# Optimization experiments

Measured on AMD Instinct MI355X. Metric: run time of the kernel, lower is better.

The kernel has to match this reference:

```python
import jax, jax.numpy as jnp
import numpy as np
import math

EMBED = 512
HEADS = 2
HEAD_DIM = EMBED // HEADS
EPS = 1e-5

def layer_norm(x, g, b):
    mu = jnp.mean(x, axis=-1, keepdims=True)
    var = jnp.var(x, axis=-1, keepdims=True)
    return (x - mu) * jax.lax.rsqrt(var + EPS) * g + b

def setup_inputs() -> dict:
    key = jax.random.key(0)
    ks = jax.random.split(key, 16)
    s = 0.02
    inp = {
        "text_embeds": jax.random.normal(ks[0], (128, 32, EMBED), jnp.float32),
        "video_embeds": jax.random.normal(ks[1], (64, 12, EMBED), jnp.float32),
        "ln1_g": jnp.ones((EMBED,), jnp.float32),
        "ln1_b": jnp.zeros((EMBED,), jnp.float32),
        "Wq": jax.random.normal(ks[2], (EMBED, EMBED), jnp.float32) * s,
        "bq": jnp.zeros((EMBED,), jnp.float32),
        "Wk": jax.random.normal(ks[3], (EMBED, EMBED), jnp.float32) * s,
        "bk": jnp.zeros((EMBED,), jnp.float32),
        "Wv": jax.random.normal(ks[4], (EMBED, EMBED), jnp.float32) * s,
        "bv": jnp.zeros((EMBED,), jnp.float32),
        "Wo": jax.random.normal(ks[5], (EMBED, EMBED), jnp.float32) * s,
        "bo": jnp.zeros((EMBED,), jnp.float32),
        "Wl": jax.random.normal(ks[6], (EMBED, EMBED), jnp.float32) * s,
        "bl": jnp.zeros((EMBED,), jnp.float32),
        "ln2_g": jnp.ones((EMBED,), jnp.float32),
        "ln2_b": jnp.zeros((EMBED,), jnp.float32),
        "ln3_g": jnp.ones((EMBED,), jnp.float32),
        "ln3_b": jnp.zeros((EMBED,), jnp.float32),
    }
    return inp

def reference(text_embeds, video_embeds, ln1_g, ln1_b, Wq, bq, Wk, bk, Wv, bv,
              Wo, bo, Wl, bl, ln2_g, ln2_b, ln3_g, ln3_b):
    # shared layer_norm1 on both modalities
    t = layer_norm(text_embeds, ln1_g, ln1_b)    # [T, Nw, E]
    vd = layer_norm(video_embeds, ln1_g, ln1_b)  # [V, F, E]
    T, Nw, _ = t.shape
    V, Fr, _ = vd.shape
    q = (t @ Wq.T + bq).reshape(T, Nw, HEADS, HEAD_DIM)   # bthd
    k = (vd @ Wk.T + bk).reshape(V, Fr, HEADS, HEAD_DIM)  # avhd
    v = (vd @ Wv.T + bv).reshape(V, Fr, HEADS, HEAD_DIM)  # avhd
    # cross-modal outer-product attention logits: [V, T, H, F, Nw]
    logits = jnp.einsum('avhd,bthd->abhvt', k, q) / math.sqrt(HEAD_DIM)
    weights = jax.nn.softmax(logits, axis=3)  # softmax over frames
    attn = jnp.einsum('avhd,abhvt->abhtd', v, weights)  # [V, T, H, Nw, D]
    attn = attn.transpose(0, 1, 3, 2, 4).reshape(V, T, Nw, EMBED)
    attn = attn.mean(axis=0)                    # [T, Nw, E]
    o = attn @ Wo.T + bo
    o = layer_norm(o, ln2_g, ln2_b)
    lin = o @ Wl.T + bl  # dropout is identity in eval mode
    out = layer_norm(o + lin, ln3_g, ln3_b)
    return out
```

## Files before the change

kernel.cpp:

```cpp
#include <hip/hip_runtime.h>
#include <math.h>

#define EMBED 512
#define HD 256
#define FR 12
#define NV 64
#define NT_TOK 4096
#define NV_TOK 768

typedef __attribute__((ext_vector_type(8))) short short8;
typedef __attribute__((ext_vector_type(4))) float f32x4;

__device__ __forceinline__ unsigned short f2bf(float f) {
  unsigned int u = __float_as_uint(f);
  u += 0x7FFFu + ((u >> 16) & 1u);
  return (unsigned short)(u >> 16);
}
__device__ __forceinline__ float bf2f(unsigned short h) {
  return __uint_as_float(((unsigned int)h) << 16);
}
__device__ __forceinline__ void async_cp16(void* lds, const void* g) {
  __builtin_amdgcn_global_load_lds(
      (const __attribute__((address_space(1))) void*)g,
      (__attribute__((address_space(3))) void*)lds, 16, 0, 0);
}

__global__ __launch_bounds__(256) void ln_kernel(
    const float* __restrict__ x, const float* __restrict__ res,
    const float* __restrict__ g, const float* __restrict__ b,
    float* __restrict__ outf, unsigned short* __restrict__ outb) {
  int row = blockIdx.x;
  int t = threadIdx.x;
  const float* xr = x + (size_t)row * EMBED;
  float v0 = xr[t];
  float v1 = xr[t + 256];
  if (res != nullptr) {
    const float* rr = res + (size_t)row * EMBED;
    v0 += rr[t];
    v1 += rr[t + 256];
  }
  float s = v0 + v1;
  float s2 = v0 * v0 + v1 * v1;
  #pragma unroll
  for (int off = 32; off > 0; off >>= 1) {
    s += __shfl_down(s, off, 64);
    s2 += __shfl_down(s2, off, 64);
  }
  __shared__ float ss[4], ss2[4];
  __shared__ float mean_s, rstd_s;
  int wid = t >> 6;
  if ((t & 63) == 0) { ss[wid] = s; ss2[wid] = s2; }
  __syncthreads();
  if (t == 0) {
    float a = ss[0] + ss[1] + ss[2] + ss[3];
    float a2 = ss2[0] + ss2[1] + ss2[2] + ss2[3];
    float mean = a * (1.0f / EMBED);
    float var = a2 * (1.0f / EMBED) - mean * mean;
    mean_s = mean;
    rstd_s = rsqrtf(var + 1e-5f);
  }
  __syncthreads();
  float mean = mean_s, rstd = rstd_s;
  float y0 = (v0 - mean) * rstd * g[t] + b[t];
  float y1 = (v1 - mean) * rstd * g[t + 256] + b[t + 256];
  if (outf != nullptr) {
    float* orow = outf + (size_t)row * EMBED;
    orow[t] = y0;
    orow[t + 256] = y1;
  }
  if (outb != nullptr) {
    unsigned short* orow = outb + (size_t)row * EMBED;
    orow[t] = f2bf(y0);
    orow[t + 256] = f2bf(y1);
  }
}

template <bool OUT_BF, bool BIAS>
__global__ __launch_bounds__(256) void gemm_mfma(
    const unsigned short* __restrict__ A, int lda, long AzS,
    const unsigned short* __restrict__ B, int ldb, long BzS,
    const float* __restrict__ bias, void* __restrict__ Cv, int ldc, long CzS,
    int K) {
  __shared__ __align__(16) unsigned short As[64 * 64];
  __shared__ __align__(16) unsigned short Bs[64 * 64];
  int tid = threadIdx.x;
  int w = tid >> 6, lane = tid & 63;
  int m0 = blockIdx.x * 64, n0 = blockIdx.y * 64;
  const unsigned short* Ab = A + (size_t)blockIdx.z * AzS;
  const unsigned short* Bb = B + (size_t)blockIdx.z * BzS;
  int wm = (w >> 1) * 32, wn = (w & 1) * 32;
  int lr = lane & 15, quad = lane >> 4;

  int s0 = lane, s1 = 64 + lane;
  int row0 = (w << 4) + (s0 >> 3), c0l = s0 & 7, c0g = c0l ^ (row0 & 7);
  int row1 = (w << 4) + (s1 >> 3), c1l = s1 & 7, c1g = c1l ^ (row1 & 7);

  f32x4 acc[2][2] = {};
  for (int k0 = 0; k0 < K; k0 += 64) {
    __syncthreads();
    async_cp16(&As[row0 * 64 + c0l * 8], Ab + (size_t)(m0 + row0) * lda + k0 + c0g * 8);
    async_cp16(&As[row1 * 64 + c1l * 8], Ab + (size_t)(m0 + row1) * lda + k0 + c1g * 8);
    async_cp16(&Bs[row0 * 64 + c0l * 8], Bb + (size_t)(n0 + row0) * ldb + k0 + c0g * 8);
    async_cp16(&Bs[row1 * 64 + c1l * 8], Bb + (size_t)(n0 + row1) * ldb + k0 + c1g * 8);
    __syncthreads();
    #pragma unroll
    for (int kk = 0; kk < 2; ++kk) {
      int sw = ((kk * 4 + quad) ^ (lr & 7)) * 8;
      short8 a0 = *(const short8*)&As[(wm + lr) * 64 + sw];
      short8 a1 = *(const short8*)&As[(wm + 16 + lr) * 64 + sw];
      short8 b0 = *(const short8*)&Bs[(wn + lr) * 64 + sw];
      short8 b1 = *(const short8*)&Bs[(wn + 16 + lr) * 64 + sw];
      acc[0][0] = __builtin_amdgcn_mfma_f32_16x16x32_bf16(a0, b0, acc[0][0], 0, 0, 0);
      acc[0][1] = __builtin_amdgcn_mfma_f32_16x16x32_bf16(a0, b1, acc[0][1], 0, 0, 0);
      acc[1][0] = __builtin_amdgcn_mfma_f32_16x16x32_bf16(a1, b0, acc[1][0], 0, 0, 0);
      acc[1][1] = __builtin_amdgcn_mfma_f32_16x16x32_bf16(a1, b1, acc[1][1], 0, 0, 0);
    }
  }
  long cz = (long)blockIdx.z * CzS;
  #pragma unroll
  for (int im = 0; im < 2; ++im) {
    #pragma unroll
    for (int in = 0; in < 2; ++in) {
      int col = n0 + wn + in * 16 + lr;
      float bv = BIAS ? bias[col] : 0.0f;
      int rbase = m0 + wm + im * 16 + quad * 4;
      #pragma unroll
      for (int r = 0; r < 4; ++r) {
        float v = acc[im][in][r] + bv;
        if (OUT_BF)
          ((unsigned short*)Cv)[cz + (size_t)(rbase + r) * ldc + col] = f2bf(v);
        else
          ((float*)Cv)[cz + (size_t)(rbase + r) * ldc + col] = v;
      }
    }
  }
}

__global__ __launch_bounds__(256) void cvt5_kernel(
    const float* __restrict__ w0, const float* __restrict__ w1,
    const float* __restrict__ w2, const float* __restrict__ w3,
    const float* __restrict__ w4, unsigned short* __restrict__ out) {
  int i = blockIdx.x * 256 + threadIdx.x;
  const float* srcs[5] = {w0, w1, w2, w3, w4};
  const float* src = srcs[i >> 16];
  float4 v = ((const float4*)src)[i & 65535];
  uint2 o;
  o.x = (unsigned)f2bf(v.x) | ((unsigned)f2bf(v.y) << 16);
  o.y = (unsigned)f2bf(v.z) | ((unsigned)f2bf(v.w) << 16);
  ((uint2*)out)[i] = o;
}

__global__ __launch_bounds__(256) void softmax12_kernel(unsigned short* __restrict__ S) {
  int gi = blockIdx.x * 256 + threadIdx.x;
  uint2* p = (uint2*)(S + (size_t)gi * 12);
  uint2 u0 = p[0], u1 = p[1], u2 = p[2];
  float v[12];
  v[0] = bf2f(u0.x & 0xffff); v[1] = bf2f(u0.x >> 16);
  v[2] = bf2f(u0.y & 0xffff); v[3] = bf2f(u0.y >> 16);
  v[4] = bf2f(u1.x & 0xffff); v[5] = bf2f(u1.x >> 16);
  v[6] = bf2f(u1.y & 0xffff); v[7] = bf2f(u1.y >> 16);
  v[8] = bf2f(u2.x & 0xffff); v[9] = bf2f(u2.x >> 16);
  v[10] = bf2f(u2.y & 0xffff); v[11] = bf2f(u2.y >> 16);
  float m = -1e30f;
  #pragma unroll
  for (int f = 0; f < FR; ++f) { v[f] *= 0.0625f; m = fmaxf(m, v[f]); }
  float s = 0.f;
  #pragma unroll
  for (int f = 0; f < FR; ++f) { v[f] = __expf(v[f] - m); s += v[f]; }
  float inv = (1.0f / NV) / s;
  unsigned short w[12];
  #pragma unroll
  for (int f = 0; f < FR; ++f) w[f] = f2bf(v[f] * inv);
  uint2 o0, o1, o2;
  o0.x = (unsigned)w[0] | ((unsigned)w[1] << 16);
  o0.y = (unsigned)w[2] | ((unsigned)w[3] << 16);
  o1.x = (unsigned)w[4] | ((unsigned)w[5] << 16);
  o1.y = (unsigned)w[6] | ((unsigned)w[7] << 16);
  o2.x = (unsigned)w[8] | ((unsigned)w[9] << 16);
  o2.y = (unsigned)w[10] | ((unsigned)w[11] << 16);
  p[0] = o0; p[1] = o1; p[2] = o2;
}

__global__ __launch_bounds__(256) void transpose_kernel(
    const unsigned short* __restrict__ V, unsigned short* __restrict__ Vt) {
  __shared__ unsigned short tile[32][34];
  int x = threadIdx.x & 31, y = threadIdx.x >> 5;
  int t0 = blockIdx.x * 32, n0 = blockIdx.y * 32;
  #pragma unroll
  for (int i = 0; i < 4; ++i)
    tile[y + i * 8][x] = V[(size_t)(t0 + y + i * 8) * EMBED + n0 + x];
  __syncthreads();
  #pragma unroll
  for (int i = 0; i < 4; ++i)
    Vt[(size_t)(n0 + y + i * 8) * NV_TOK + t0 + x] = tile[x][y + i * 8];
}

extern "C" void kernel_launch(void* const* d_in, const int* in_sizes, int n_in,
                              void* d_out, int out_size, void* d_ws, size_t ws_size,
                              hipStream_t stream) {
  (void)in_sizes; (void)n_in; (void)out_size; (void)ws_size;
  const float* text  = (const float*)d_in[0];
  const float* video = (const float*)d_in[1];
  const float* ln1_g = (const float*)d_in[2];
  const float* ln1_b = (const float*)d_in[3];
  const float* Wq = (const float*)d_in[4];
  const float* bq = (const float*)d_in[5];
  const float* Wk = (const float*)d_in[6];
  const float* bk = (const float*)d_in[7];
  const float* Wv = (const float*)d_in[8];
  const float* bv = (const float*)d_in[9];
  const float* Wo = (const float*)d_in[10];
  const float* bo = (const float*)d_in[11];
  const float* Wl = (const float*)d_in[12];
  const float* bl = (const float*)d_in[13];
  const float* ln2_g = (const float*)d_in[14];
  const float* ln2_b = (const float*)d_in[15];
  const float* ln3_g = (const float*)d_in[16];
  const float* ln3_b = (const float*)d_in[17];
  float* out = (float*)d_out;

  char* base = (char*)d_ws;
  unsigned short* Wbf   = (unsigned short*)base;
  unsigned short* Wq_bf = Wbf + 0 * 262144;
  unsigned short* Wk_bf = Wbf + 1 * 262144;
  unsigned short* Wv_bf = Wbf + 2 * 262144;
  unsigned short* Wo_bf = Wbf + 3 * 262144;
  unsigned short* Wl_bf = Wbf + 4 * 262144;
  unsigned short* Vt    = (unsigned short*)(base + 2621440);
  char* big = base + 3407872;
  unsigned short* Q_bf   = (unsigned short*)(big + 0);
  unsigned short* K_bf   = (unsigned short*)(big + 4194304);
  unsigned short* S      = (unsigned short*)(big + 4980736);
  unsigned short* tn_bf  = (unsigned short*)(big + 17563648);
  unsigned short* vn_bf  = (unsigned short*)(big + 21757952);
  unsigned short* V_bf   = (unsigned short*)(big + 22544384);
  unsigned short* att_bf = (unsigned short*)(big + 17563648);
  float*          Ob     = (float*)(big + 4980736);
  float*          o2f    = (float*)(big + 13369344);
  unsigned short* o2_bf  = (unsigned short*)(big + 21757952);
  float*          lin    = (float*)(big + 0);

  cvt5_kernel<<<1280, 256, 0, stream>>>(Wq, Wk, Wv, Wo, Wl, Wbf);
  ln_kernel<<<NT_TOK, 256, 0, stream>>>(text, nullptr, ln1_g, ln1_b, nullptr, tn_bf);
  ln_kernel<<<NV_TOK, 256, 0, stream>>>(video, nullptr, ln1_g, ln1_b, nullptr, vn_bf);

  gemm_mfma<true, true><<<dim3(64, 8, 1), 256, 0, stream>>>(
      tn_bf, EMBED, 0, Wq_bf, EMBED, 0, bq, Q_bf, EMBED, 0, EMBED);
  gemm_mfma<true, true><<<dim3(12, 8, 1), 256, 0, stream>>>(
      vn_bf, EMBED, 0, Wk_bf, EMBED, 0, bk, K_bf, EMBED, 0, EMBED);
  gemm_mfma<true, true><<<dim3(12, 8, 1), 256, 0, stream>>>(
      vn_bf, EMBED, 0, Wv_bf, EMBED, 0, bv, V_bf, EMBED, 0, EMBED);
  transpose_kernel<<<dim3(24, 16), 256, 0, stream>>>(V_bf, Vt);

  gemm_mfma<true, false><<<dim3(64, 12, 2), 256, 0, stream>>>(
      Q_bf, EMBED, HD, K_bf, EMBED, HD, nullptr, S, NV_TOK, (long)NT_TOK * NV_TOK, HD);
  softmax12_kernel<<<2048, 256, 0, stream>>>(S);
  gemm_mfma<true, false><<<dim3(64, 4, 2), 256, 0, stream>>>(
      S, NV_TOK, (long)NT_TOK * NV_TOK, Vt, NV_TOK, (long)HD * NV_TOK, nullptr,
      att_bf, EMBED, HD, NV_TOK);

  gemm_mfma<false, true><<<dim3(64, 8, 1), 256, 0, stream>>>(
      att_bf, EMBED, 0, Wo_bf, EMBED, 0, bo, Ob, EMBED, 0, EMBED);
  ln_kernel<<<NT_TOK, 256, 0, stream>>>(Ob, nullptr, ln2_g, ln2_b, o2f, o2_bf);
  gemm_mfma<false, true><<<dim3(64, 8, 1), 256, 0, stream>>>(
      o2_bf, EMBED, 0, Wl_bf, EMBED, 0, bl, lin, EMBED, 0, EMBED);
  ln_kernel<<<NT_TOK, 256, 0, stream>>>(o2f, lin, ln3_g, ln3_b, out, nullptr);
}
```

Measured before the change: 183.9 us.

## Fuse prep and QKV launches, write V transposed, enlarge GEMM tiles to 128x64

Merges the weight conversion and both layer norms into one prep kernel, and merges the Q, K and V projections into one grid-partitioned kernel. The V projection now writes its output directly in transposed layout, which removes the separate transpose kernel. All GEMMs move from 64x64 to 128x64 block tiles, so each block reuses its B tile across more rows. The aims are fewer launches and less tile reload traffic, at the cost of fewer blocks per grid and more registers per thread.

```diff
diff --git a/kernel.cpp b/kernel.cpp
--- a/kernel.cpp
+++ b/kernel.cpp
@@ -11,13 +11,13 @@
 typedef __attribute__((ext_vector_type(8))) short short8;
 typedef __attribute__((ext_vector_type(4))) float f32x4;
 
-__device__ __forceinline__ unsigned short f2bf(float f) {
+__device__ __forceinline__ unsigned int f2bf(float f) {
   unsigned int u = __float_as_uint(f);
   u += 0x7FFFu + ((u >> 16) & 1u);
-  return (unsigned short)(u >> 16);
-}
-__device__ __forceinline__ float bf2f(unsigned short h) {
-  return __uint_as_float(((unsigned int)h) << 16);
+  return u >> 16;
+}
+__device__ __forceinline__ float bf2f(unsigned int h) {
+  return __uint_as_float(h << 16);
 }
 __device__ __forceinline__ void async_cp16(void* lds, const void* g) {
   __builtin_amdgcn_global_load_lds(
@@ -25,20 +25,154 @@
       (__attribute__((address_space(3))) void*)lds, 16, 0, 0);
 }
 
-__global__ __launch_bounds__(256) void ln_kernel(
-    const float* __restrict__ x, const float* __restrict__ res,
+__device__ __forceinline__ void gemm_core(
+    const unsigned short* __restrict__ Ab, int lda,
+    const unsigned short* __restrict__ Bb, int ldb,
+    int m0, int n0, int K,
+    unsigned short* As, unsigned short* Bs, f32x4 acc[4][2]) {
+  int tid = threadIdx.x;
+  int w = tid >> 6, lane = tid & 63;
+  int lr = lane & 15, quad = lane >> 4;
+  int wm = (w >> 1) * 64, wn = (w & 1) * 32;
+  int rowA[4], cgA[4], rowB[2], cgB[2];
+  #pragma unroll
+  for (int i = 0; i < 4; ++i) {
+    int s = tid + i * 256;
+    rowA[i] = s >> 3;
+    cgA[i] = (s & 7) ^ (rowA[i] & 7);
+  }
+  #pragma unroll
+  for (int i = 0; i < 2; ++i) {
+    int s = tid + i * 256;
+    rowB[i] = s >> 3;
+    cgB[i] = (s & 7) ^ (rowB[i] & 7);
+  }
+  for (int k0 = 0; k0 < K; k0 += 64) {
+    __syncthreads();
+    #pragma unroll
+    for (int i = 0; i < 4; ++i)
+      async_cp16(&As[(tid + i * 256) * 8],
+                 Ab + (size_t)(m0 + rowA[i]) * lda + k0 + cgA[i] * 8);
+    #pragma unroll
+    for (int i = 0; i < 2; ++i)
+      async_cp16(&Bs[(tid + i * 256) * 8],
+                 Bb + (size_t)(n0 + rowB[i]) * ldb + k0 + cgB[i] * 8);
+    __syncthreads();
+    #pragma unroll
+    for (int kk = 0; kk < 2; ++kk) {
+      int sw = ((kk * 4 + quad) ^ (lr & 7)) * 8;
+      short8 b0 = *(const short8*)&Bs[(wn + lr) * 64 + sw];
+      short8 b1 = *(const short8*)&Bs[(wn + 16 + lr) * 64 + sw];
+      #pragma unroll
+      for (int i = 0; i < 4; ++i) {
+        short8 a = *(const short8*)&As[(wm + i * 16 + lr) * 64 + sw];
+        acc[i][0] = __builtin_amdgcn_mfma_f32_16x16x32_bf16(a, b0, acc[i][0], 0, 0, 0);
+        acc[i][1] = __builtin_amdgcn_mfma_f32_16x16x32_bf16(a, b1, acc[i][1], 0, 0, 0);
+      }
+    }
+  }
+}
+
+template <bool OUT_BF, bool BIAS>
+__global__ __launch_bounds__(256) void gemm128(
+    const unsigned short* __restrict__ A, int lda, long AzS,
+    const unsigned short* __restrict__ B, int ldb, long BzS,
+    const float* __restrict__ bias, void* __restrict__ Cv, int ldc, long CzS,
+    int K) {
+  __shared__ __align__(16) unsigned short As[128 * 64];
+  __shared__ __align__(16) unsigned short Bs[64 * 64];
+  f32x4 acc[4][2] = {};
+  const unsigned short* Ab = A + (size_t)blockIdx.z * AzS;
+  const unsigned short* Bb = B + (size_t)blockIdx.z * BzS;
+  int m0 = blockIdx.x * 128, n0 = blockIdx.y * 64;
+  gemm_core(Ab, lda, Bb, ldb, m0, n0, K, As, Bs, acc);
+  int w = threadIdx.x >> 6, lane = threadIdx.x & 63;
+  int lr = lane & 15, quad = lane >> 4;
+  int wm = (w >> 1) * 64, wn = (w & 1) * 32;
+  long cz = (long)blockIdx.z * CzS;
+  #pragma unroll
+  for (int j = 0; j < 2; ++j) {
+    int col = n0 + wn + j * 16 + lr;
+    float bv = BIAS ? bias[col] : 0.0f;
+    #pragma unroll
+    for (int i = 0; i < 4; ++i) {
+      int rbase = m0 + wm + i * 16 + quad * 4;
+      #pragma unroll
+      for (int r = 0; r < 4; ++r) {
+        float v = acc[i][j][r] + bv;
+        if (OUT_BF)
+          ((unsigned short*)Cv)[cz + (size_t)(rbase + r) * ldc + col] =
+              (unsigned short)f2bf(v);
+        else
+          ((float*)Cv)[cz + (size_t)(rbase + r) * ldc + col] = v;
+      }
+    }
+  }
+}
+
+__global__ __launch_bounds__(256) void qkv_kernel(
+    const unsigned short* __restrict__ tn, const unsigned short* __restrict__ vn,
+    const unsigned short* __restrict__ Wq, const unsigned short* __restrict__ Wk,
+    const unsigned short* __restrict__ Wv,
+    const float* __restrict__ bq, const float* __restrict__ bk,
+    const float* __restrict__ bv,
+    unsigned short* __restrict__ Q, unsigned short* __restrict__ Kout,
+    unsigned short* __restrict__ Vt) {
+  __shared__ __align__(16) unsigned short As[128 * 64];
+  __shared__ __align__(16) unsigned short Bs[64 * 64];
+  int bid = blockIdx.x;
+  const unsigned short *Ap, *Bp;
+  const float* bias;
+  unsigned short* outp = nullptr;
+  int m0, n0, mode;
+  if (bid < 256) {
+    Ap = tn; Bp = Wq; bias = bq; outp = Q;
+    m0 = (bid >> 3) * 128; n0 = (bid & 7) * 64; mode = 0;
+  } else if (bid < 304) {
+    int i = bid - 256;
+    Ap = vn; Bp = Wk; bias = bk; outp = Kout;
+    m0 = (i >> 3) * 128; n0 = (i & 7) * 64; mode = 0;
+  } else {
+    int i = bid - 304;
+    Ap = vn; Bp = Wv; bias = bv;
+    m0 = (i >> 3) * 128; n0 = (i & 7) * 64; mode = 1;
+  }
+  f32x4 acc[4][2] = {};
+  gemm_core(Ap, EMBED, Bp, EMBED, m0, n0, EMBED, As, Bs, acc);
+  int w = threadIdx.x >> 6, lane = threadIdx.x & 63;
+  int lr = lane & 15, quad = lane >> 4;
+  int wm = (w >> 1) * 64, wn = (w & 1) * 32;
+  #pragma unroll
+  for (int j = 0; j < 2; ++j) {
+    int col = n0 + wn + j * 16 + lr;
+    float bvv = bias[col];
+    #pragma unroll
+    for (int i = 0; i < 4; ++i) {
+      int rbase = m0 + wm + i * 16 + quad * 4;
+      if (mode == 0) {
+        #pragma unroll
+        for (int r = 0; r < 4; ++r)
+          outp[(size_t)(rbase + r) * EMBED + col] =
+              (unsigned short)f2bf(acc[i][j][r] + bvv);
+      } else {
+        ushort4 pk;
+        pk.x = (unsigned short)f2bf(acc[i][j][0] + bvv);
+        pk.y = (unsigned short)f2bf(acc[i][j][1] + bvv);
+        pk.z = (unsigned short)f2bf(acc[i][j][2] + bvv);
+        pk.w = (unsigned short)f2bf(acc[i][j][3] + bvv);
+        *(ushort4*)&Vt[(size_t)col * NV_TOK + rbase] = pk;
+      }
+    }
+  }
+}
+
+__device__ __forceinline__ void ln_row(
+    const float* __restrict__ xr, const float* __restrict__ rr,
     const float* __restrict__ g, const float* __restrict__ b,
     float* __restrict__ outf, unsigned short* __restrict__ outb) {
-  int row = blockIdx.x;
   int t = threadIdx.x;
-  const float* xr = x + (size_t)row * EMBED;
-  float v0 = xr[t];
-  float v1 = xr[t + 256];
-  if (res != nullptr) {
-    const float* rr = res + (size_t)row * EMBED;
-    v0 += rr[t];
-    v1 += rr[t + 256];
-  }
+  float v0 = xr[t], v1 = xr[t + 256];
+  if (rr != nullptr) { v0 += rr[t]; v1 += rr[t + 256]; }
   float s = v0 + v1;
   float s2 = v0 * v0 + v1 * v1;
   #pragma unroll
@@ -63,91 +197,49 @@
   float mean = mean_s, rstd = rstd_s;
   float y0 = (v0 - mean) * rstd * g[t] + b[t];
   float y1 = (v1 - mean) * rstd * g[t + 256] + b[t + 256];
-  if (outf != nullptr) {
-    float* orow = outf + (size_t)row * EMBED;
-    orow[t] = y0;
-    orow[t + 256] = y1;
-  }
+  if (outf != nullptr) { outf[t] = y0; outf[t + 256] = y1; }
   if (outb != nullptr) {
-    unsigned short* orow = outb + (size_t)row * EMBED;
-    orow[t] = f2bf(y0);
-    orow[t + 256] = f2bf(y1);
-  }
-}
-
-template <bool OUT_BF, bool BIAS>
-__global__ __launch_bounds__(256) void gemm_mfma(
-    const unsigned short* __restrict__ A, int lda, long AzS,
-    const unsigned short* __restrict__ B, int ldb, long BzS,
-    const float* __restrict__ bias, void* __restrict__ Cv, int ldc, long CzS,
-    int K) {
-  __shared__ __align__(16) unsigned short As[64 * 64];
-  __shared__ __align__(16) unsigned short Bs[64 * 64];
-  int tid = threadIdx.x;
-  int w = tid >> 6, lane = tid & 63;
-  int m0 = blockIdx.x * 64, n0 = blockIdx.y * 64;
-  const unsigned short* Ab = A + (size_t)blockIdx.z * AzS;
-  const unsigned short* Bb = B + (size_t)blockIdx.z * BzS;
-  int wm = (w >> 1) * 32, wn = (w & 1) * 32;
-  int lr = lane & 15, quad = lane >> 4;
-
-  int s0 = lane, s1 = 64 + lane;
-  int row0 = (w << 4) + (s0 >> 3), c0l = s0 & 7, c0g = c0l ^ (row0 & 7);
-  int row1 = (w << 4) + (s1 >> 3), c1l = s1 & 7, c1g = c1l ^ (row1 & 7);
-
-  f32x4 acc[2][2] = {};
-  for (int k0 = 0; k0 < K; k0 += 64) {
-    __syncthreads();
-    async_cp16(&As[row0 * 64 + c0l * 8], Ab + (size_t)(m0 + row0) * lda + k0 + c0g * 8);
-    async_cp16(&As[row1 * 64 + c1l * 8], Ab + (size_t)(m0 + row1) * lda + k0 + c1g * 8);
-    async_cp16(&Bs[row0 * 64 + c0l * 8], Bb + (size_t)(n0 + row0) * ldb + k0 + c0g * 8);
-    async_cp16(&Bs[row1 * 64 + c1l * 8], Bb + (size_t)(n0 + row1) * ldb + k0 + c1g * 8);
-    __syncthreads();
-    #pragma unroll
-    for (int kk = 0; kk < 2; ++kk) {
-      int sw = ((kk * 4 + quad) ^ (lr & 7)) * 8;
-      short8 a0 = *(const short8*)&As[(wm + lr) * 64 + sw];
-      short8 a1 = *(const short8*)&As[(wm + 16 + lr) * 64 + sw];
-      short8 b0 = *(const short8*)&Bs[(wn + lr) * 64 + sw];
-      short8 b1 = *(const short8*)&Bs[(wn + 16 + lr) * 64 + sw];
-      acc[0][0] = __builtin_amdgcn_mfma_f32_16x16x32_bf16(a0, b0, acc[0][0], 0, 0, 0);
-      acc[0][1] = __builtin_amdgcn_mfma_f32_16x16x32_bf16(a0, b1, acc[0][1], 0, 0, 0);
-      acc[1][0] = __builtin_amdgcn_mfma_f32_16x16x32_bf16(a1, b0, acc[1][0], 0, 0, 0);
-      acc[1][1] = __builtin_amdgcn_mfma_f32_16x16x32_bf16(a1, b1, acc[1][1], 0, 0, 0);
-    }
-  }
-  long cz = (long)blockIdx.z * CzS;
-  #pragma unroll
-  for (int im = 0; im < 2; ++im) {
-    #pragma unroll
-    for (int in = 0; in < 2; ++in) {
-      int col = n0 + wn + in * 16 + lr;
-      float bv = BIAS ? bias[col] : 0.0f;
-      int rbase = m0 + wm + im * 16 + quad * 4;
-      #pragma unroll
-      for (int r = 0; r < 4; ++r) {
-        float v = acc[im][in][r] + bv;
-        if (OUT_BF)
-          ((unsigned short*)Cv)[cz + (size_t)(rbase + r) * ldc + col] = f2bf(v);
-        else
-          ((float*)Cv)[cz + (size_t)(rbase + r) * ldc + col] = v;
-      }
-    }
-  }
-}
-
-__global__ __launch_bounds__(256) void cvt5_kernel(
-    const float* __restrict__ w0, const float* __restrict__ w1,
-    const float* __restrict__ w2, const float* __restrict__ w3,
-    const float* __restrict__ w4, unsigned short* __restrict__ out) {
-  int i = blockIdx.x * 256 + threadIdx.x;
-  const float* srcs[5] = {w0, w1, w2, w3, w4};
-  const float* src = srcs[i >> 16];
-  float4 v = ((const float4*)src)[i & 65535];
-  uint2 o;
-  o.x = (unsigned)f2bf(v.x) | ((unsigned)f2bf(v.y) << 16);
-  o.y = (unsigned)f2bf(v.z) | ((unsigned)f2bf(v.w) << 16);
-  ((uint2*)out)[i] = o;
+    outb[t] = (unsigned short)f2bf(y0);
+    outb[t + 256] = (unsigned short)f2bf(y1);
+  }
+}
+
+__global__ __launch_bounds__(256) void ln_kernel(
+    const float* __restrict__ x, const float* __restrict__ res,
+    const float* __restrict__ g, const float* __restrict__ b,
+    float* __restrict__ outf, unsigned short* __restrict__ outb) {
+  size_t row = blockIdx.x;
+  ln_row(x + row * EMBED, res ? res + row * EMBED : nullptr, g, b,
+         outf ? outf + row * EMBED : nullptr,
+         outb ? outb + row * EMBED : nullptr);
+}
+
+__global__ __launch_bounds__(256) void prep_kernel(
+    const float* __restrict__ text, const float* __restrict__ video,
+    const float* __restrict__ g, const float* __restrict__ b,
+    const float* __restrict__ Wq, const float* __restrict__ Wk,
+    const float* __restrict__ Wv, const float* __restrict__ Wo,
+    const float* __restrict__ Wl, unsigned short* __restrict__ Wbf,
+    unsigned short* __restrict__ tn, unsigned short* __restrict__ vn) {
+  int bid = blockIdx.x;
+  if (bid < 1280) {
+    int i = bid * 256 + threadIdx.x;
+    const float* srcs[5] = {Wq, Wk, Wv, Wo, Wl};
+    const float* src = srcs[i >> 16];
+    float4 v = ((const float4*)src)[i & 65535];
+    uint2 o;
+    o.x = f2bf(v.x) | (f2bf(v.y) << 16);
+    o.y = f2bf(v.z) | (f2bf(v.w) << 16);
+    ((uint2*)Wbf)[i] = o;
+    return;
+  }
+  if (bid < 1280 + NT_TOK) {
+    size_t row = bid - 1280;
+    ln_row(text + row * EMBED, nullptr, g, b, nullptr, tn + row * EMBED);
+  } else {
+    size_t row = bid - (1280 + NT_TOK);
+    ln_row(video + row * EMBED, nullptr, g, b, nullptr, vn + row * EMBED);
+  }
 }
 
 __global__ __launch_bounds__(256) void softmax12_kernel(unsigned short* __restrict__ S) {
@@ -168,31 +260,14 @@
   #pragma unroll
   for (int f = 0; f < FR; ++f) { v[f] = __expf(v[f] - m); s += v[f]; }
   float inv = (1.0f / NV) / s;
-  unsigned short w[12];
+  unsigned int w[12];
   #pragma unroll
   for (int f = 0; f < FR; ++f) w[f] = f2bf(v[f] * inv);
   uint2 o0, o1, o2;
-  o0.x = (unsigned)w[0] | ((unsigned)w[1] << 16);
-  o0.y = (unsigned)w[2] | ((unsigned)w[3] << 16);
-  o1.x = (unsigned)w[4] | ((unsigned)w[5] << 16);
-  o1.y = (unsigned)w[6] | ((unsigned)w[7] << 16);
-  o2.x = (unsigned)w[8] | ((unsigned)w[9] << 16);
-  o2.y = (unsigned)w[10] | ((unsigned)w[11] << 16);
+  o0.x = w[0] | (w[1] << 16);  o0.y = w[2] | (w[3] << 16);
+  o1.x = w[4] | (w[5] << 16);  o1.y = w[6] | (w[7] << 16);
+  o2.x = w[8] | (w[9] << 16);  o2.y = w[10] | (w[11] << 16);
   p[0] = o0; p[1] = o1; p[2] = o2;
-}
-
-__global__ __launch_bounds__(256) void transpose_kernel(
-    const unsigned short* __restrict__ V, unsigned short* __restrict__ Vt) {
-  __shared__ unsigned short tile[32][34];
-  int x = threadIdx.x & 31, y = threadIdx.x >> 5;
-  int t0 = blockIdx.x * 32, n0 = blockIdx.y * 32;
-  #pragma unroll
-  for (int i = 0; i < 4; ++i)
-    tile[y + i * 8][x] = V[(size_t)(t0 + y + i * 8) * EMBED + n0 + x];
-  __syncthreads();
-  #pragma unroll
-  for (int i = 0; i < 4; ++i)
-    Vt[(size_t)(n0 + y + i * 8) * NV_TOK + t0 + x] = tile[x][y + i * 8];
 }
 
 extern "C" void kernel_launch(void* const* d_in, const int* in_sizes, int n_in,
@@ -233,36 +308,30 @@
   unsigned short* S      = (unsigned short*)(big + 4980736);
   unsigned short* tn_bf  = (unsigned short*)(big + 17563648);
   unsigned short* vn_bf  = (unsigned short*)(big + 21757952);
-  unsigned short* V_bf   = (unsigned short*)(big + 22544384);
   unsigned short* att_bf = (unsigned short*)(big + 17563648);
   float*          Ob     = (float*)(big + 4980736);
   float*          o2f    = (float*)(big + 13369344);
   unsigned short* o2_bf  = (unsigned short*)(big + 21757952);
   float*          lin    = (float*)(big + 0);
 
-  cvt5_kernel<<<1280, 256, 0, stream>>>(Wq, Wk, Wv, Wo, Wl, Wbf);
-  ln_kernel<<<NT_TOK, 256, 0, stream>>>(text, nullptr, ln1_g, ln1_b, nullptr, tn_bf);
-  ln_kernel<<<NV_TOK, 256, 0, stream>>>(video, nullptr, ln1_g, ln1_b, nullptr, vn_bf);
-
-  gemm_mfma<true, true><<<dim3(64, 8, 1), 256, 0, stream>>>(
-      tn_bf, EMBED, 0, Wq_bf, EMBED, 0, bq, Q_bf, EMBED, 0, EMBED);
-  gemm_mfma<true, true><<<dim3(12, 8, 1), 256, 0, stream>>>(
-      vn_bf, EMBED, 0, Wk_bf, EMBED, 0, bk, K_bf, EMBED, 0, EMBED);
-  gemm_mfma<true, true><<<dim3(12, 8, 1), 256, 0, stream>>>(
-      vn_bf, EMBED, 0, Wv_bf, EMBED, 0, bv, V_bf, EMBED, 0, EMBED);
-  transpose_kernel<<<dim3(24, 16), 256, 0, stream>>>(V_bf, Vt);
-
-  gemm_mfma<true, false><<<dim3(64, 12, 2), 256, 0, stream>>>(
-      Q_bf, EMBED, HD, K_bf, EMBED, HD, nullptr, S, NV_TOK, (long)NT_TOK * NV_TOK, HD);
+  prep_kernel<<<1280 + NT_TOK + NV_TOK, 256, 0, stream>>>(
+      text, video, ln1_g, ln1_b, Wq, Wk, Wv, Wo, Wl, Wbf, tn_bf, vn_bf);
+
+  qkv_kernel<<<352, 256, 0, stream>>>(tn_bf, vn_bf, Wq_bf, Wk_bf, Wv_bf,
+                                      bq, bk, bv, Q_bf, K_bf, Vt);
+
+  gemm128<true, false><<<dim3(32, 12, 2), 256, 0, stream>>>(
+      Q_bf, EMBED, HD, K_bf, EMBED, HD, nullptr, S, NV_TOK,
+      (long)NT_TOK * NV_TOK, HD);
   softmax12_kernel<<<2048, 256, 0, stream>>>(S);
-  gemm_mfma<true, false><<<dim3(64, 4, 2), 256, 0, stream>>>(
+  gemm128<true, false><<<dim3(32, 4, 2), 256, 0, stream>>>(
       S, NV_TOK, (long)NT_TOK * NV_TOK, Vt, NV_TOK, (long)HD * NV_TOK, nullptr,
       att_bf, EMBED, HD, NV_TOK);
 
-  gemm_mfma<false, true><<<dim3(64, 8, 1), 256, 0, stream>>>(
+  gemm128<false, true><<<dim3(32, 8, 1), 256, 0, stream>>>(
       att_bf, EMBED, 0, Wo_bf, EMBED, 0, bo, Ob, EMBED, 0, EMBED);
   ln_kernel<<<NT_TOK, 256, 0, stream>>>(Ob, nullptr, ln2_g, ln2_b, o2f, o2_bf);
-  gemm_mfma<false, true><<<dim3(64, 8, 1), 256, 0, stream>>>(
+  gemm128<false, true><<<dim3(32, 8, 1), 256, 0, stream>>>(
       o2_bf, EMBED, 0, Wl_bf, EMBED, 0, bl, lin, EMBED, 0, EMBED);
   ln_kernel<<<NT_TOK, 256, 0, stream>>>(o2f, lin, ln3_g, ln3_b, out, nullptr);
 }
```

Result: faster. 176.2 us (-4.2%).

## Fuse all stages into one persistent megakernel with grid barriers

Applied to the files above, without the earlier changes.

Replaces the chain of separate kernel launches with a single persistent kernel of 256 blocks that runs every stage in sequence, separated by atomic grid-wide barriers. The GEMM tiles grow to 128x128 with double-buffered async LDS loads. The V projection writes its transposed output directly, and softmax stages through LDS. This removes launch gaps and the separate transpose pass. In exchange, some phases leave most blocks idle (only 128 or 176 of 256 work), and correctness depends on all blocks being co-resident for the spin barriers.

```diff
diff --git a/kernel.cpp b/kernel.cpp
--- a/kernel.cpp
+++ b/kernel.cpp
@@ -7,17 +7,22 @@
 #define NV 64
 #define NT_TOK 4096
 #define NV_TOK 768
+#define NBLK 256
+#define MAGIC 0x13579BDF
+
+#define WAIT_VM4 0x0F74
+#define WAIT_VM0 0x0F70
 
 typedef __attribute__((ext_vector_type(8))) short short8;
 typedef __attribute__((ext_vector_type(4))) float f32x4;
 
-__device__ __forceinline__ unsigned short f2bf(float f) {
+__device__ __forceinline__ unsigned int f2bf(float f) {
   unsigned int u = __float_as_uint(f);
   u += 0x7FFFu + ((u >> 16) & 1u);
-  return (unsigned short)(u >> 16);
-}
-__device__ __forceinline__ float bf2f(unsigned short h) {
-  return __uint_as_float(((unsigned int)h) << 16);
+  return u >> 16;
+}
+__device__ __forceinline__ float bf2f(unsigned int h) {
+  return __uint_as_float(h << 16);
 }
 __device__ __forceinline__ void async_cp16(void* lds, const void* g) {
   __builtin_amdgcn_global_load_lds(
@@ -25,244 +30,346 @@
       (__attribute__((address_space(3))) void*)lds, 16, 0, 0);
 }
 
-__global__ __launch_bounds__(256) void ln_kernel(
-    const float* __restrict__ x, const float* __restrict__ res,
+__device__ __forceinline__ void gbar(int* sync, int idx) {
+  __syncthreads();
+  if (threadIdx.x == 0) {
+    __threadfence();
+    __hip_atomic_fetch_add(&sync[idx], 1, __ATOMIC_ACQ_REL,
+                           __HIP_MEMORY_SCOPE_AGENT);
+    while (__hip_atomic_load(&sync[idx], __ATOMIC_ACQUIRE,
+                             __HIP_MEMORY_SCOPE_AGENT) < NBLK)
+      __builtin_amdgcn_s_sleep(8);
+    __threadfence();
+  }
+  __syncthreads();
+}
+
+template <int MODE>
+__device__ void gemm_tile(
+    const unsigned short* __restrict__ Ab, int lda,
+    const unsigned short* __restrict__ Bb, int ldb,
+    const float* __restrict__ bias, void* __restrict__ Cv, int ldc,
+    int m0, int n0, int K,
+    unsigned short (*As)[8192], unsigned short (*Bs)[8192]) {
+  int tid = threadIdx.x;
+  int w = tid >> 6, lane = tid & 63;
+  int lr = lane & 15, quad = lane >> 4;
+  int wm = (w & 3) * 32, wn = (w >> 2) * 64;
+  int rowS[2], cgS[2];
+  #pragma unroll
+  for (int i = 0; i < 2; ++i) {
+    int s = tid + i * 512;
+    rowS[i] = s >> 3; cgS[i] = (s & 7) ^ (rowS[i] & 7);
+  }
+  f32x4 acc[2][4] = {};
+  int nk = K >> 6;
+  #pragma unroll
+  for (int i = 0; i < 2; ++i) {
+    async_cp16(&As[0][(tid + i * 512) * 8],
+               Ab + (size_t)(m0 + rowS[i]) * lda + cgS[i] * 8);
+    async_cp16(&Bs[0][(tid + i * 512) * 8],
+               Bb + (size_t)(n0 + rowS[i]) * ldb + cgS[i] * 8);
+  }
+  for (int k = 0; k < nk; ++k) {
+    int cur = k & 1;
+    __builtin_amdgcn_s_barrier();
+    if (k + 1 < nk) {
+      int nxt = cur ^ 1, koff = (k + 1) << 6;
+      #pragma unroll
+      for (int i = 0; i < 2; ++i) {
+        async_cp16(&As[nxt][(tid + i * 512) * 8],
+                   Ab + (size_t)(m0 + rowS[i]) * lda + koff + cgS[i] * 8);
+        async_cp16(&Bs[nxt][(tid + i * 512) * 8],
+                   Bb + (size_t)(n0 + rowS[i]) * ldb + koff + cgS[i] * 8);
+      }
+      __builtin_amdgcn_s_waitcnt(WAIT_VM4);
+    } else {
+      __builtin_amdgcn_s_waitcnt(WAIT_VM0);
+    }
+    __builtin_amdgcn_s_barrier();
+    #pragma unroll
+    for (int kk = 0; kk < 2; ++kk) {
+      int sw = ((kk * 4 + quad) ^ (lr & 7)) * 8;
+      short8 a0 = *(const short8*)&As[cur][(wm + lr) * 64 + sw];
+      short8 a1 = *(const short8*)&As[cur][(wm + 16 + lr) * 64 + sw];
+      short8 b0 = *(const short8*)&Bs[cur][(wn + lr) * 64 + sw];
+      short8 b1 = *(const short8*)&Bs[cur][(wn + 16 + lr) * 64 + sw];
+      short8 b2 = *(const short8*)&Bs[cur][(wn + 32 + lr) * 64 + sw];
+      short8 b3 = *(const short8*)&Bs[cur][(wn + 48 + lr) * 64 + sw];
+      acc[0][0] = __builtin_amdgcn_mfma_f32_16x16x32_bf16(a0, b0, acc[0][0], 0, 0, 0);
+      acc[0][1] = __builtin_amdgcn_mfma_f32_16x16x32_bf16(a0, b1, acc[0][1], 0, 0, 0);
+      acc[0][2] = __builtin_amdgcn_mfma_f32_16x16x32_bf16(a0, b2, acc[0][2], 0, 0, 0);
+      acc[0][3] = __builtin_amdgcn_mfma_f32_16x16x32_bf16(a0, b3, acc[0][3], 0, 0, 0);
+      acc[1][0] = __builtin_amdgcn_mfma_f32_16x16x32_bf16(a1, b0, acc[1][0], 0, 0, 0);
+      acc[1][1] = __builtin_amdgcn_mfma_f32_16x16x32_bf16(a1, b1, acc[1][1], 0, 0, 0);
+      acc[1][2] = __builtin_amdgcn_mfma_f32_16x16x32_bf16(a1, b2, acc[1][2], 0, 0, 0);
+      acc[1][3] = __builtin_amdgcn_mfma_f32_16x16x32_bf16(a1, b3, acc[1][3], 0, 0, 0);
+    }
+  }
+  #pragma unroll
+  for (int j = 0; j < 4; ++j) {
+    int col = n0 + wn + j * 16 + lr;
+    float bv = bias ? bias[col] : 0.0f;
+    #pragma unroll
+    for (int i = 0; i < 2; ++i) {
+      int rbase = m0 + wm + i * 16 + quad * 4;
+      if (MODE == 2) {
+        ushort4 pk;
+        pk.x = (unsigned short)f2bf(acc[i][j][0] + bv);
+        pk.y = (unsigned short)f2bf(acc[i][j][1] + bv);
+        pk.z = (unsigned short)f2bf(acc[i][j][2] + bv);
+        pk.w = (unsigned short)f2bf(acc[i][j][3] + bv);
+        *(ushort4*)&((unsigned short*)Cv)[(size_t)col * ldc + rbase] = pk;
+      } else {
+        #pragma unroll
+        for (int r = 0; r < 4; ++r) {
+          float v = acc[i][j][r] + bv;
+          if (MODE == 0)
+            ((unsigned short*)Cv)[(size_t)(rbase + r) * ldc + col] =
+                (unsigned short)f2bf(v);
+          else
+            ((float*)Cv)[(size_t)(rbase + r) * ldc + col] = v;
+        }
+      }
+    }
+  }
+}
+
+__device__ __forceinline__ void ln_row512(
+    const float* __restrict__ xr, const float* __restrict__ rr,
     const float* __restrict__ g, const float* __restrict__ b,
-    float* __restrict__ outf, unsigned short* __restrict__ outb) {
-  int row = blockIdx.x;
+    float* __restrict__ outf, unsigned short* __restrict__ outb,
+    float* sbuf) {
   int t = threadIdx.x;
-  const float* xr = x + (size_t)row * EMBED;
-  float v0 = xr[t];
-  float v1 = xr[t + 256];
-  if (res != nullptr) {
-    const float* rr = res + (size_t)row * EMBED;
-    v0 += rr[t];
-    v1 += rr[t + 256];
-  }
-  float s = v0 + v1;
-  float s2 = v0 * v0 + v1 * v1;
+  float v = xr[t];
+  if (rr != nullptr) v += rr[t];
+  float s = v, s2 = v * v;
   #pragma unroll
   for (int off = 32; off > 0; off >>= 1) {
     s += __shfl_down(s, off, 64);
     s2 += __shfl_down(s2, off, 64);
   }
-  __shared__ float ss[4], ss2[4];
-  __shared__ float mean_s, rstd_s;
   int wid = t >> 6;
-  if ((t & 63) == 0) { ss[wid] = s; ss2[wid] = s2; }
+  __syncthreads();
+  if ((t & 63) == 0) { sbuf[wid] = s; sbuf[8 + wid] = s2; }
   __syncthreads();
   if (t == 0) {
-    float a = ss[0] + ss[1] + ss[2] + ss[3];
-    float a2 = ss2[0] + ss2[1] + ss2[2] + ss2[3];
+    float a = 0.f, a2 = 0.f;
+    #pragma unroll
+    for (int i = 0; i < 8; ++i) { a += sbuf[i]; a2 += sbuf[8 + i]; }
     float mean = a * (1.0f / EMBED);
     float var = a2 * (1.0f / EMBED) - mean * mean;
-    mean_s = mean;
-    rstd_s = rsqrtf(var + 1e-5f);
-  }
-  __syncthreads();
-  float mean = mean_s, rstd = rstd_s;
-  float y0 = (v0 - mean) * rstd * g[t] + b[t];
-  float y1 = (v1 - mean) * rstd * g[t + 256] + b[t + 256];
-  if (outf != nullptr) {
-    float* orow = outf + (size_t)row * EMBED;
-    orow[t] = y0;
-    orow[t + 256] = y1;
-  }
-  if (outb != nullptr) {
-    unsigned short* orow = outb + (size_t)row * EMBED;
-    orow[t] = f2bf(y0);
-    orow[t + 256] = f2bf(y1);
-  }
-}
-
-template <bool OUT_BF, bool BIAS>
-__global__ __launch_bounds__(256) void gemm_mfma(
-    const unsigned short* __restrict__ A, int lda, long AzS,
-    const unsigned short* __restrict__ B, int ldb, long BzS,
-    const float* __restrict__ bias, void* __restrict__ Cv, int ldc, long CzS,
-    int K) {
-  __shared__ __align__(16) unsigned short As[64 * 64];
-  __shared__ __align__(16) unsigned short Bs[64 * 64];
-  int tid = threadIdx.x;
-  int w = tid >> 6, lane = tid & 63;
-  int m0 = blockIdx.x * 64, n0 = blockIdx.y * 64;
-  const unsigned short* Ab = A + (size_t)blockIdx.z * AzS;
-  const unsigned short* Bb = B + (size_t)blockIdx.z * BzS;
-  int wm = (w >> 1) * 32, wn = (w & 1) * 32;
-  int lr = lane & 15, quad = lane >> 4;
-
-  int s0 = lane, s1 = 64 + lane;
-  int row0 = (w << 4) + (s0 >> 3), c0l = s0 & 7, c0g = c0l ^ (row0 & 7);
-  int row1 = (w << 4) + (s1 >> 3), c1l = s1 & 7, c1g = c1l ^ (row1 & 7);
-
-  f32x4 acc[2][2] = {};
-  for (int k0 = 0; k0 < K; k0 += 64) {
-    __syncthreads();
-    async_cp16(&As[row0 * 64 + c0l * 8], Ab + (size_t)(m0 + row0) * lda + k0 + c0g * 8);
-    async_cp16(&As[row1 * 64 + c1l * 8], Ab + (size_t)(m0 + row1) * lda + k0 + c1g * 8);
-    async_cp16(&Bs[row0 * 64 + c0l * 8], Bb + (size_t)(n0 + row0) * ldb + k0 + c0g * 8);
-    async_cp16(&Bs[row1 * 64 + c1l * 8], Bb + (size_t)(n0 + row1) * ldb + k0 + c1g * 8);
-    __syncthreads();
-    #pragma unroll
-    for (int kk = 0; kk < 2; ++kk) {
-      int sw = ((kk * 4 + quad) ^ (lr & 7)) * 8;
-      short8 a0 = *(const short8*)&As[(wm + lr) * 64 + sw];
-      short8 a1 = *(const short8*)&As[(wm + 16 + lr) * 64 + sw];
-      short8 b0 = *(const short8*)&Bs[(wn + lr) * 64 + sw];
-      short8 b1 = *(const short8*)&Bs[(wn + 16 + lr) * 64 + sw];
-      acc[0][0] = __builtin_amdgcn_mfma_f32_16x16x32_bf16(a0, b0, acc[0][0], 0, 0, 0);
-      acc[0][1] = __builtin_amdgcn_mfma_f32_16x16x32_bf16(a0, b1, acc[0][1], 0, 0, 0);
-      acc[1][0] = __builtin_amdgcn_mfma_f32_16x16x32_bf16(a1, b0, acc[1][0], 0, 0, 0);
-      acc[1][1] = __builtin_amdgcn_mfma_f32_16x16x32_bf16(a1, b1, acc[1][1], 0, 0, 0);
-    }
-  }
-  long cz = (long)blockIdx.z * CzS;
-  #pragma unroll
-  for (int im = 0; im < 2; ++im) {
-    #pragma unroll
-    for (int in = 0; in < 2; ++in) {
-      int col = n0 + wn + in * 16 + lr;
-      float bv = BIAS ? bias[col] : 0.0f;
-      int rbase = m0 + wm + im * 16 + quad * 4;
-      #pragma unroll
-      for (int r = 0; r < 4; ++r) {
-        float v = acc[im][in][r] + bv;
-        if (OUT_BF)
-          ((unsigned short*)Cv)[cz + (size_t)(rbase + r) * ldc + col] = f2bf(v);
-        else
-          ((float*)Cv)[cz + (size_t)(rbase + r) * ldc + col] = v;
-      }
-    }
-  }
-}
-
-__global__ __launch_bounds__(256) void cvt5_kernel(
-    const float* __restrict__ w0, const float* __restrict__ w1,
-    const float* __restrict__ w2, const float* __restrict__ w3,
-    const float* __restrict__ w4, unsigned short* __restrict__ out) {
-  int i = blockIdx.x * 256 + threadIdx.x;
-  const float* srcs[5] = {w0, w1, w2, w3, w4};
-  const float* src = srcs[i >> 16];
-  float4 v = ((const float4*)src)[i & 65535];
-  uint2 o;
-  o.x = (unsigned)f2bf(v.x) | ((unsigned)f2bf(v.y) << 16);
-  o.y = (unsigned)f2bf(v.z) | ((unsigned)f2bf(v.w) << 16);
-  ((uint2*)out)[i] = o;
-}
-
-__global__ __launch_bounds__(256) void softmax12_kernel(unsigned short* __restrict__ S) {
-  int gi = blockIdx.x * 256 + threadIdx.x;
-  uint2* p = (uint2*)(S + (size_t)gi * 12);
-  uint2 u0 = p[0], u1 = p[1], u2 = p[2];
-  float v[12];
-  v[0] = bf2f(u0.x & 0xffff); v[1] = bf2f(u0.x >> 16);
-  v[2] = bf2f(u0.y & 0xffff); v[3] = bf2f(u0.y >> 16);
-  v[4] = bf2f(u1.x & 0xffff); v[5] = bf2f(u1.x >> 16);
-  v[6] = bf2f(u1.y & 0xffff); v[7] = bf2f(u1.y >> 16);
-  v[8] = bf2f(u2.x & 0xffff); v[9] = bf2f(u2.x >> 16);
-  v[10] = bf2f(u2.y & 0xffff); v[11] = bf2f(u2.y >> 16);
-  float m = -1e30f;
-  #pragma unroll
-  for (int f = 0; f < FR; ++f) { v[f] *= 0.0625f; m = fmaxf(m, v[f]); }
-  float s = 0.f;
-  #pragma unroll
-  for (int f = 0; f < FR; ++f) { v[f] = __expf(v[f] - m); s += v[f]; }
-  float inv = (1.0f / NV) / s;
-  unsigned short w[12];
-  #pragma unroll
-  for (int f = 0; f < FR; ++f) w[f] = f2bf(v[f] * inv);
-  uint2 o0, o1, o2;
-  o0.x = (unsigned)w[0] | ((unsigned)w[1] << 16);
-  o0.y = (unsigned)w[2] | ((unsigned)w[3] << 16);
-  o1.x = (unsigned)w[4] | ((unsigned)w[5] << 16);
-  o1.y = (unsigned)w[6] | ((unsigned)w[7] << 16);
-  o2.x = (unsigned)w[8] | ((unsigned)w[9] << 16);
-  o2.y = (unsigned)w[10] | ((unsigned)w[11] << 16);
-  p[0] = o0; p[1] = o1; p[2] = o2;
-}
-
-__global__ __launch_bounds__(256) void transpose_kernel(
-    const unsigned short* __restrict__ V, unsigned short* __restrict__ Vt) {
-  __shared__ unsigned short tile[32][34];
-  int x = threadIdx.x & 31, y = threadIdx.x >> 5;
-  int t0 = blockIdx.x * 32, n0 = blockIdx.y * 32;
-  #pragma unroll
-  for (int i = 0; i < 4; ++i)
-    tile[y + i * 8][x] = V[(size_t)(t0 + y + i * 8) * EMBED + n0 + x];
-  __syncthreads();
-  #pragma unroll
-  for (int i = 0; i < 4; ++i)
-    Vt[(size_t)(n0 + y + i * 8) * NV_TOK + t0 + x] = tile[x][y + i * 8];
-}
-
-extern "C" void kernel_launch(void* const* d_in, const int* in_sizes, int n_in,
-                              void* d_out, int out_size, void* d_ws, size_t ws_size,
-                              hipStream_t stream) {
-  (void)in_sizes; (void)n_in; (void)out_size; (void)ws_size;
-  const float* text  = (const float*)d_in[0];
-  const float* video = (const float*)d_in[1];
-  const float* ln1_g = (const float*)d_in[2];
-  const float* ln1_b = (const float*)d_in[3];
-  const float* Wq = (const float*)d_in[4];
-  const float* bq = (const float*)d_in[5];
-  const float* Wk = (const float*)d_in[6];
-  const float* bk = (const float*)d_in[7];
-  const float* Wv = (const float*)d_in[8];
-  const float* bv = (const float*)d_in[9];
-  const float* Wo = (const float*)d_in[10];
-  const float* bo = (const float*)d_in[11];
-  const float* Wl = (const float*)d_in[12];
-  const float* bl = (const float*)d_in[13];
-  const float* ln2_g = (const float*)d_in[14];
-  const float* ln2_b = (const float*)d_in[15];
-  const float* ln3_g = (const float*)d_in[16];
-  const float* ln3_b = (const float*)d_in[17];
-  float* out = (float*)d_out;
-
-  char* base = (char*)d_ws;
-  unsigned short* Wbf   = (unsigned short*)base;
+    sbuf[16] = mean;
+    sbuf[17] = rsqrtf(var + 1e-5f);
+  }
+  __syncthreads();
+  float mean = sbuf[16], rstd = sbuf[17];
+  float y = (v - mean) * rstd * g[t] + b[t];
+  if (outf != nullptr) outf[t] = y;
+  if (outb != nullptr) outb[t] = (unsigned short)f2bf(y);
+}
+
+__global__ __launch_bounds__(512, 2) void mega(
+    const float* __restrict__ text, const float* __restrict__ video,
+    const float* __restrict__ ln1_g, const float* __restrict__ ln1_b,
+    const float* __restrict__ Wq, const float* __restrict__ bq,
+    const float* __restrict__ Wk, const float* __restrict__ bk,
+    const float* __restrict__ Wv, const float* __restrict__ bv,
+    const float* __restrict__ Wo, const float* __restrict__ bo,
+    const float* __restrict__ Wl, const float* __restrict__ bl,
+    const float* __restrict__ ln2_g, const float* __restrict__ ln2_b,
+    const float* __restrict__ ln3_g, const float* __restrict__ ln3_b,
+    float* __restrict__ out, char* __restrict__ ws) {
+  __shared__ __align__(16) unsigned short As[2][8192];
+  __shared__ __align__(16) unsigned short Bs[2][8192];
+  __shared__ __align__(16) char scratch[20480];
+
+  unsigned short* Wbf = (unsigned short*)ws;
   unsigned short* Wq_bf = Wbf + 0 * 262144;
   unsigned short* Wk_bf = Wbf + 1 * 262144;
   unsigned short* Wv_bf = Wbf + 2 * 262144;
   unsigned short* Wo_bf = Wbf + 3 * 262144;
   unsigned short* Wl_bf = Wbf + 4 * 262144;
-  unsigned short* Vt    = (unsigned short*)(base + 2621440);
-  char* big = base + 3407872;
-  unsigned short* Q_bf   = (unsigned short*)(big + 0);
-  unsigned short* K_bf   = (unsigned short*)(big + 4194304);
-  unsigned short* S      = (unsigned short*)(big + 4980736);
-  unsigned short* tn_bf  = (unsigned short*)(big + 17563648);
-  unsigned short* vn_bf  = (unsigned short*)(big + 21757952);
-  unsigned short* V_bf   = (unsigned short*)(big + 22544384);
-  unsigned short* att_bf = (unsigned short*)(big + 17563648);
-  float*          Ob     = (float*)(big + 4980736);
-  float*          o2f    = (float*)(big + 13369344);
-  unsigned short* o2_bf  = (unsigned short*)(big + 21757952);
-  float*          lin    = (float*)(big + 0);
-
-  cvt5_kernel<<<1280, 256, 0, stream>>>(Wq, Wk, Wv, Wo, Wl, Wbf);
-  ln_kernel<<<NT_TOK, 256, 0, stream>>>(text, nullptr, ln1_g, ln1_b, nullptr, tn_bf);
-  ln_kernel<<<NV_TOK, 256, 0, stream>>>(video, nullptr, ln1_g, ln1_b, nullptr, vn_bf);
-
-  gemm_mfma<true, true><<<dim3(64, 8, 1), 256, 0, stream>>>(
-      tn_bf, EMBED, 0, Wq_bf, EMBED, 0, bq, Q_bf, EMBED, 0, EMBED);
-  gemm_mfma<true, true><<<dim3(12, 8, 1), 256, 0, stream>>>(
-      vn_bf, EMBED, 0, Wk_bf, EMBED, 0, bk, K_bf, EMBED, 0, EMBED);
-  gemm_mfma<true, true><<<dim3(12, 8, 1), 256, 0, stream>>>(
-      vn_bf, EMBED, 0, Wv_bf, EMBED, 0, bv, V_bf, EMBED, 0, EMBED);
-  transpose_kernel<<<dim3(24, 16), 256, 0, stream>>>(V_bf, Vt);
-
-  gemm_mfma<true, false><<<dim3(64, 12, 2), 256, 0, stream>>>(
-      Q_bf, EMBED, HD, K_bf, EMBED, HD, nullptr, S, NV_TOK, (long)NT_TOK * NV_TOK, HD);
-  softmax12_kernel<<<2048, 256, 0, stream>>>(S);
-  gemm_mfma<true, false><<<dim3(64, 4, 2), 256, 0, stream>>>(
-      S, NV_TOK, (long)NT_TOK * NV_TOK, Vt, NV_TOK, (long)HD * NV_TOK, nullptr,
-      att_bf, EMBED, HD, NV_TOK);
-
-  gemm_mfma<false, true><<<dim3(64, 8, 1), 256, 0, stream>>>(
-      att_bf, EMBED, 0, Wo_bf, EMBED, 0, bo, Ob, EMBED, 0, EMBED);
-  ln_kernel<<<NT_TOK, 256, 0, stream>>>(Ob, nullptr, ln2_g, ln2_b, o2f, o2_bf);
-  gemm_mfma<false, true><<<dim3(64, 8, 1), 256, 0, stream>>>(
-      o2_bf, EMBED, 0, Wl_bf, EMBED, 0, bl, lin, EMBED, 0, EMBED);
-  ln_kernel<<<NT_TOK, 256, 0, stream>>>(o2f, lin, ln3_g, ln3_b, out, nullptr);
-}
+  unsigned short* Vt = (unsigned short*)(ws + 2621440);
+  char* big = ws + 3407872;
+  unsigned short* Q_bf  = (unsigned short*)(big + 0);
+  unsigned short* K_bf  = (unsigned short*)(big + 4194304);
+  unsigned short* S     = (unsigned short*)(big + 4980736);
+  unsigned short* tn_bf = (unsigned short*)(big + 17563648);
+  unsigned short* vn_bf = (unsigned short*)(big + 21757952);
+  unsigned short* att_bf = tn_bf;
+  float* Ob  = (float*)(big + 4980736);
+  float* o2f = (float*)(big + 13369344);
+  unsigned short* o2_bf = vn_bf;
+  float* lin = (float*)(big + 0);
+  int* sync = (int*)(ws + 29360128);
+
+  int bid = blockIdx.x, tid = threadIdx.x;
+
+  if (bid == 0) {
+    if (tid < 15) sync[tid] = 0;
+    __syncthreads();
+    if (tid == 0) {
+      __threadfence();
+      __hip_atomic_store(&sync[15], MAGIC, __ATOMIC_RELEASE,
+                         __HIP_MEMORY_SCOPE_AGENT);
+    }
+    __syncthreads();
+  } else {
+    if (tid == 0)
+      while (__hip_atomic_load(&sync[15], __ATOMIC_ACQUIRE,
+                               __HIP_MEMORY_SCOPE_AGENT) != (int)MAGIC)
+        __builtin_amdgcn_s_sleep(8);
+    __syncthreads();
+  }
+
+  {
+    int gtid = bid * 512 + tid;
+    for (int i = gtid; i < 327680; i += 131072) {
+      const float* src = (i < 65536) ? Wq
+                       : (i < 131072) ? Wk
+                       : (i < 196608) ? Wv
+                       : (i < 262144) ? Wo : Wl;
+      float4 v = ((const float4*)src)[i & 65535];
+      uint2 o;
+      o.x = f2bf(v.x) | (f2bf(v.y) << 16);
+      o.y = f2bf(v.z) | (f2bf(v.w) << 16);
+      ((uint2*)Wbf)[i] = o;
+    }
+    float* sbuf = (float*)scratch;
+    for (int it = 0; it < 19; ++it) {
+      int r = bid + it * 256;
+      if (r < NT_TOK)
+        ln_row512(text + (size_t)r * EMBED, nullptr, ln1_g, ln1_b, nullptr,
+                  tn_bf + (size_t)r * EMBED, sbuf);
+      else
+        ln_row512(video + (size_t)(r - NT_TOK) * EMBED, nullptr, ln1_g, ln1_b,
+                  nullptr, vn_bf + (size_t)(r - NT_TOK) * EMBED, sbuf);
+    }
+  }
+  gbar(sync, 0);
+
+  {
+    int j = bid;
+    if (j < 128) {
+      int m0 = (j >> 2) * 128, n0 = (j & 3) * 128;
+      gemm_tile<0>(tn_bf, EMBED, Wq_bf, EMBED, bq, Q_bf, EMBED, m0, n0, EMBED,
+                   As, Bs);
+    } else if (j < 152) {
+      int i = j - 128;
+      int m0 = (i >> 2) * 128, n0 = (i & 3) * 128;
+      gemm_tile<0>(vn_bf, EMBED, Wk_bf, EMBED, bk, K_bf, EMBED, m0, n0, EMBED,
+                   As, Bs);
+    } else if (j < 176) {
+      int i = j - 152;
+      int m0 = (i >> 2) * 128, n0 = (i & 3) * 128;
+      gemm_tile<2>(vn_bf, EMBED, Wv_bf, EMBED, bv, Vt, NV_TOK, m0, n0, EMBED,
+                   As, Bs);
+    }
+  }
+  gbar(sync, 1);
+
+  for (int jj = bid; jj < 384; jj += 256) {
+    int h = jj / 192, i = jj % 192;
+    int m0 = (i / 6) * 128, n0 = (i % 6) * 128;
+    gemm_tile<0>(Q_bf + h * HD, EMBED, K_bf + h * HD, EMBED, nullptr,
+                 S + (size_t)h * NT_TOK * NV_TOK, NV_TOK, m0, n0, HD, As, Bs);
+  }
+  gbar(sync, 2);
+
+  {
+    uint2* sb = (uint2*)scratch;
+    for (int it = 0; it < 4; ++it) {
+      int c = bid + it * 256;
+      uint2* gp = (uint2*)S + (size_t)c * 1536;
+      __syncthreads();
+      #pragma unroll
+      for (int i = 0; i < 3; ++i) sb[tid + i * 512] = gp[tid + i * 512];
+      __syncthreads();
+      uint2 u0 = sb[tid * 3], u1 = sb[tid * 3 + 1], u2 = sb[tid * 3 + 2];
+      float v[12];
+      v[0] = bf2f(u0.x & 0xffff);  v[1] = bf2f(u0.x >> 16);
+      v[2] = bf2f(u0.y & 0xffff);  v[3] = bf2f(u0.y >> 16);
+      v[4] = bf2f(u1.x & 0xffff);  v[5] = bf2f(u1.x >> 16);
+      v[6] = bf2f(u1.y & 0xffff);  v[7] = bf2f(u1.y >> 16);
+      v[8] = bf2f(u2.x & 0xffff);  v[9] = bf2f(u2.x >> 16);
+      v[10] = bf2f(u2.y & 0xffff); v[11] = bf2f(u2.y >> 16);
+      float m = -1e30f;
+      #pragma unroll
+      for (int f = 0; f < FR; ++f) { v[f] *= 0.0625f; m = fmaxf(m, v[f]); }
+      float s = 0.f;
+      #pragma unroll
+      for (int f = 0; f < FR; ++f) { v[f] = __expf(v[f] - m); s += v[f]; }
+      float inv = (1.0f / NV) / s;
+      unsigned int wv_[12];
+      #pragma unroll
+      for (int f = 0; f < FR; ++f) wv_[f] = f2bf(v[f] * inv);
+      sb[tid * 3]     = (uint2){wv_[0] | (wv_[1] << 16), wv_[2] | (wv_[3] << 16)};
+      sb[tid * 3 + 1] = (uint2){wv_[4] | (wv_[5] << 16), wv_[6] | (wv_[7] << 16)};
+      sb[tid * 3 + 2] = (uint2){wv_[8] | (wv_[9] << 16), wv_[10] | (wv_[11] << 16)};
+      __syncthreads();
+      #pragma unroll
+      for (int i = 0; i < 3; ++i) gp[tid + i * 512] = sb[tid + i * 512];
+    }
+  }
+  gbar(sync, 3);
+
+  if (bid < 128) {
+    int h = bid >> 6, i = bid & 63;
+    int m0 = (i >> 1) * 128, n0 = (i & 1) * 128;
+    gemm_tile<0>(S + (size_t)h * NT_TOK * NV_TOK, NV_TOK,
+                 Vt + (size_t)h * HD * NV_TOK, NV_TOK, nullptr,
+                 att_bf + h * HD, EMBED, m0, n0, NV_TOK, As, Bs);
+  }
+  gbar(sync, 4);
+
+  if (bid < 128) {
+    int m0 = (bid >> 2) * 128, n0 = (bid & 3) * 128;
+    gemm_tile<1>(att_bf, EMBED, Wo_bf, EMBED, bo, Ob, EMBED, m0, n0, EMBED,
+                 As, Bs);
+  }
+  gbar(sync, 5);
+
+  {
+    float* sbuf = (float*)scratch;
+    for (int it = 0; it < 16; ++it) {
+      int r = bid + it * 256;
+      ln_row512(Ob + (size_t)r * EMBED, nullptr, ln2_g, ln2_b,
+                o2f + (size_t)r * EMBED, o2_bf + (size_t)r * EMBED, sbuf);
+    }
+  }
+  gbar(sync, 6);
+
+  if (bid < 128) {
+    int m0 = (bid >> 2) * 128, n0 = (bid & 3) * 128;
+    gemm_tile<1>(o2_bf, EMBED, Wl_bf, EMBED, bl, lin, EMBED, m0, n0, EMBED,
+                 As, Bs);
+  }
+  gbar(sync, 7);
+
+  {
+    float* sbuf = (float*)scratch;
+    for (int it = 0; it < 16; ++it) {
+      int r = bid + it * 256;
+      ln_row512(o2f + (size_t)r * EMBED, lin + (size_t)r * EMBED, ln3_g, ln3_b,
+                out + (size_t)r * EMBED, nullptr, sbuf);
+    }
+  }
+}
+
+extern "C" void kernel_launch(void* const* d_in, const int* in_sizes, int n_in,
+                              void* d_out, int out_size, void* d_ws, size_t ws_size,
+                              hipStream_t stream) {
+  (void)in_sizes; (void)n_in; (void)out_size; (void)ws_size;
+  mega<<<NBLK, 512, 0, stream>>>(
+      (const float*)d_in[0], (const float*)d_in[1],
+      (const float*)d_in[2], (const float*)d_in[3],
+      (const float*)d_in[4], (const float*)d_in[5],
+      (const float*)d_in[6], (const float*)d_in[7],
+      (const float*)d_in[8], (const float*)d_in[9],
+      (const float*)d_in[10], (const float*)d_in[11],
+      (const float*)d_in[12], (const float*)d_in[13],
+      (const float*)d_in[14], (const float*)d_in[15],
+      (const float*)d_in[16], (const float*)d_in[17],
+      (float*)d_out, (char*)d_ws);
+}
```

After: 513.1 us. 179% more time.
